# Performance work log

Measured on AMD Instinct MI355X. Metric: run time of the kernel, lower is better.

## Reference

```python
import jax, jax.numpy as jnp
from jax import lax
import numpy as np

H = 200           # mpnn_hidden_size
DEPTH = 3         # mpnn_depth
ATOM_FDIM = 39
BOND_FDIM = 11
B, NA, NB = 128, 48, 96   # molecules, atoms/mol, bonds/mol (padded fixed size)
L, VOCAB = 1000, 26       # protein length, amino-acid vocab
KERNALS = [3, 5, 7]
PROT_FILTERS = [50, 96, 128, 200]
FC_DIMS = [400, 200, 100, 1]


def setup_inputs() -> dict:
    key = jax.random.key(0)
    ks = jax.random.split(key, 32)
    s = 0.05
    inp = {}
    inp["fatoms"] = jax.random.normal(ks[0], (B, NA, ATOM_FDIM), jnp.float32)
    inp["fbonds"] = jax.random.normal(ks[1], (B, NB, ATOM_FDIM + BOND_FDIM), jnp.float32)
    inp["agraph"] = jax.random.randint(ks[2], (B, NA, 6), 0, NB)
    inp["bgraph"] = jax.random.randint(ks[3], (B, NB, 6), 0, NB)
    inp["protein_seq"] = jax.random.randint(ks[4], (B, L), 0, VOCAB)
    # MPNN weights (stored as (in, out) matrices; W_i and W_h have no bias)
    inp["W_i"] = jax.random.normal(ks[5], (ATOM_FDIM + BOND_FDIM, H), jnp.float32) * s
    inp["W_h"] = jax.random.normal(ks[6], (H, H), jnp.float32) * s
    inp["W_o_w"] = jax.random.normal(ks[7], (ATOM_FDIM + H, H), jnp.float32) * s
    inp["W_o_b"] = jax.random.normal(ks[8], (H,), jnp.float32) * s
    # protein embedding + CNN
    inp["embed_protein"] = jax.random.normal(ks[9], (VOCAB, PROT_FILTERS[0]), jnp.float32) * s
    for i, k in enumerate(KERNALS):
        inp[f"conv{i}_w"] = jax.random.normal(ks[10 + 2 * i], (PROT_FILTERS[i + 1], PROT_FILTERS[i], k), jnp.float32) * s
        inp[f"conv{i}_b"] = jax.random.normal(ks[11 + 2 * i], (PROT_FILTERS[i + 1],), jnp.float32) * s
    # CPI fc head 400 -> 200 -> 100 -> 1
    for i in range(3):
        inp[f"fc{i}_w"] = jax.random.normal(ks[16 + 2 * i], (FC_DIMS[i], FC_DIMS[i + 1]), jnp.float32) * s
        inp[f"fc{i}_b"] = jax.random.normal(ks[17 + 2 * i], (FC_DIMS[i + 1],), jnp.float32) * s
    return inp


def reference(fatoms, fbonds, agraph, bgraph, protein_seq,
              W_i, W_h, W_o_w, W_o_b, embed_protein,
              conv0_w, conv0_b, conv1_w, conv1_b, conv2_w, conv2_b,
              fc0_w, fc0_b, fc1_w, fc1_b, fc2_w, fc2_b):
    # ---- MPNN over all molecules (vmapped single_molecule_forward) ----
    def mol(fa, fb, ag, bg):
        binput = fb @ W_i                      # (NB, H)
        message = jax.nn.relu(binput)
        for _ in range(DEPTH - 1):
            nei = message[bg].sum(axis=1)      # gather (NB,6,H) -> sum -> (NB,H)
            message = jax.nn.relu(binput + nei @ W_h)
        nei = message[ag].sum(axis=1)          # (NA, H)
        atom_h = jax.nn.relu(jnp.concatenate([fa, nei], axis=1) @ W_o_w + W_o_b)
        return atom_h.mean(axis=0)             # (H,)

    embeddings = jax.vmap(mol)(fatoms, fbonds, agraph, bgraph)  # (B, H)

    # ---- protein CNN tower ----
    pv = embed_protein[protein_seq]            # (B, L, 50)
    pv = pv.transpose(0, 2, 1)                 # (B, 50, L)
    for w, b, k in ((conv0_w, conv0_b, KERNALS[0]),
                    (conv1_w, conv1_b, KERNALS[1]),
                    (conv2_w, conv2_b, KERNALS[2])):
        pv = lax.conv_general_dilated(pv, w, window_strides=(1,),
                                      padding=[(k // 2, k // 2)],
                                      dimension_numbers=("NCH", "OIH", "NCH"))
        pv = jax.nn.relu(pv + b[None, :, None])
    protein_vector = pv.max(axis=2)            # adaptive_max_pool1d(out=1) -> (B, 200)

    # ---- CPI fc head ----
    x = jnp.concatenate([embeddings, protein_vector], axis=1)  # (B, 400)
    x = jax.nn.relu(x @ fc0_w + fc0_b)
    x = jax.nn.relu(x @ fc1_w + fc1_b)
    x = x @ fc2_w + fc2_b
    return x                                   # (B, 1)
```

## Files before the change

### kernel.cpp

```cpp
#include <hip/hip_runtime.h>
#include <hip/hip_bf16.h>
#include <cstddef>

#define H 200
#define NA 48
#define NBB 96
#define BATCH 128
#define AFD 39
#define BFD 50
#define LP 1000
#define CATD (AFD + H)
#define BIPB 16
#define VOCAB 26
#define EROW 56

typedef unsigned short ushort_t;
typedef __bf16 bf16x8 __attribute__((ext_vector_type(8)));
typedef float f32x16 __attribute__((ext_vector_type(16)));
typedef unsigned uint32x4 __attribute__((ext_vector_type(4)));

union U16B { uint4 u; bf16x8 b; };
static __device__ __forceinline__ bf16x8 as_bf16x8(uint4 u) { U16B x; x.u = u; return x.b; }
union U16B2 { uint32x4 u; bf16x8 b; };
static __device__ __forceinline__ bf16x8 as_bf16x8v(uint32x4 u) { U16B2 x; x.u = u; return x.b; }

static __device__ __forceinline__ ushort_t f2bf(float f) {
    union { float f; unsigned u; } a; a.f = f;
    unsigned r = (a.u + 0x7FFFu + ((a.u >> 16) & 1u)) >> 16;
    return (ushort_t)r;
}

static __device__ __forceinline__ uint32x4 gload16(const ushort_t* base, unsigned voff) {
    uint32x4 r;
    asm volatile("global_load_dwordx4 %0, %1, %2"
                 : "=&v"(r) : "v"(voff), "s"(base));
    return r;
}

template <int COUT, int CIN, int CP, int K>
static __device__ __forceinline__ void prep_one(int t, const float* __restrict__ w,
                                                ushort_t* __restrict__ Wb) {
    constexpr int NC = CP / 16;
    constexpr int NS = K * NC;
    int j = t & 7;
    int lane = (t >> 3) & 63;
    int s = (t >> 9) % NS;
    int ct = (t >> 9) / NS;
    int co = ct * 32 + (lane & 31);
    int tt = s / NC, cc = s % NC;
    int ci = cc * 16 + ((lane >> 5) & 1) * 8 + j;
    float v = 0.f;
    if (co < COUT && ci < CIN) v = w[((size_t)co * CIN + ci) * K + tt];
    Wb[t] = f2bf(v);
}

#define MNS 13
#define ANS 15
#define PREP_T0 (4 * 12 * 512)
#define PREP_T1 (PREP_T0 + 4 * 30 * 512)
#define PREP_T2 (PREP_T1 + 8 * 56 * 512)
#define PREP_T3 (PREP_T2 + 51200)
#define PREP_T4 (PREP_T3 + 8 * MNS * 512)
#define PREP_T5 (PREP_T4 + 8 * ANS * 512)
#define PREP_T6 (PREP_T5 + VOCAB * EROW)
#define PREP_T7 (PREP_T6 + 200 * 400)
#define PREP_T8 (PREP_T7 + 100 * 200)
#define PREP_BLKS ((PREP_T8 + 255) / 256)

static __device__ __forceinline__ void prep_body(
        int tid, const float* __restrict__ c0w, const float* __restrict__ c1w,
        const float* __restrict__ c2w, const float* __restrict__ Wh,
        const float* __restrict__ Wo, const float* __restrict__ emb,
        const float* __restrict__ fc0w, const float* __restrict__ fc1w,
        float* __restrict__ x,
        ushort_t* __restrict__ Wb0, ushort_t* __restrict__ Wb1,
        ushort_t* __restrict__ Wb2, ushort_t* __restrict__ Wbh,
        ushort_t* __restrict__ Wbo, ushort_t* __restrict__ embb,
        float* __restrict__ w0t, float* __restrict__ w1t) {
    if (tid < PREP_T0) prep_one<96, 50, 64, 3>(tid, c0w, Wb0);
    else if (tid < PREP_T1) prep_one<128, 96, 96, 5>(tid - PREP_T0, c1w, Wb1);
    else if (tid < PREP_T2) prep_one<200, 128, 128, 7>(tid - PREP_T1, c2w, Wb2);
    else if (tid < PREP_T3) x[tid - PREP_T2] = 0.f;
    else if (tid < PREP_T4) {
        int t = tid - PREP_T3;
        int j = t & 7;
        int lane = (t >> 3) & 63;
        int s = (t >> 9) % MNS;
        int tile = (t >> 9) / MNS;
        int co = tile * 32 + (lane & 31);
        int ci = s * 16 + ((lane >> 5) & 1) * 8 + j;
        float v = 0.f;
        if (co < H && ci < H) v = Wh[ci * H + co];
        Wbh[t] = f2bf(v);
    } else if (tid < PREP_T5) {
        int t = tid - PREP_T4;
        int j = t & 7;
        int lane = (t >> 3) & 63;
        int s = (t >> 9) % ANS;
        int tile = (t >> 9) / ANS;
        int co = tile * 32 + (lane & 31);
        int cip = s * 16 + ((lane >> 5) & 1) * 8 + j;
        float v = 0.f;
        if (co < H) {
            if (cip < 200) v = Wo[(size_t)(39 + cip) * H + co];
            else if (cip < CATD) v = Wo[(size_t)(cip - 200) * H + co];
        }
        Wbo[t] = f2bf(v);
    } else if (tid < PREP_T6) {
        int t = tid - PREP_T5;
        int s = t / EROW, cc = t - s * EROW;
        embb[t] = (cc < 50) ? f2bf(emb[(size_t)s * 50 + cc]) : (ushort_t)0;
    } else if (tid < PREP_T7) {
        int t = tid - PREP_T6;
        int co = t % 200, k = t / 200;
        w0t[(size_t)co * 400 + k] = fc0w[(size_t)k * 200 + co];
    } else if (tid < PREP_T8) {
        int t = tid - PREP_T7;
        int co = t % 100, k = t / 100;
        w1t[(size_t)co * 200 + k] = fc1w[(size_t)k * 100 + co];
    }
}

template <int CP, int K, int COUT, int CO_WAVES, int L_WAVES, bool FMAX, bool EMB>
static __device__ __forceinline__ void conv_body(
        const ushort_t* __restrict__ act, const int* __restrict__ seq,
        const ushort_t* __restrict__ embb, const ushort_t* __restrict__ Wb,
        const float* __restrict__ bias, void* __restrict__ outv,
        ushort_t* __restrict__ Xs, int bofs) {
    constexpr int NC = CP / 16;
    constexpr int NS = K * NC;
    constexpr int P = K / 2;
    constexpr int PITCH = CP + 8;
    constexpr int LTILE = 64 * L_WAVES;
    constexpr int ROWS = LTILE + K - 1;
    constexpr int CPR = CP / 8;
    constexpr int D = 4;

    int b = blockIdx.z + bofs, lb = blockIdx.x;
    int l0 = lb * LTILE;
    int tid = threadIdx.x;

    if (EMB) {
        const int* seqb = seq + (size_t)b * LP;
        for (int idx = tid; idx < ROWS * CPR; idx += 256) {
            int r = idx / CPR, c = idx % CPR;
            int l = l0 - P + r;
            uint4 v = {0u, 0u, 0u, 0u};
            if ((unsigned)l < (unsigned)LP && c < 7) {
                int s = seqb[l];
                v = *(const uint4*)(embb + (size_t)s * EROW + c * 8);
            }
            *(uint4*)(Xs + r * PITCH + c * 8) = v;
        }
    } else {
        const ushort_t* actb = act + (size_t)b * LP * CP;
        for (int idx = tid; idx < ROWS * CPR; idx += 256) {
            int r = idx / CPR, c = idx % CPR;
            int l = l0 - P + r;
            uint4 v = {0u, 0u, 0u, 0u};
            if ((unsigned)l < (unsigned)LP)
                v = *(const uint4*)(actb + ((size_t)c * LP + l) * 8);
            *(uint4*)(Xs + r * PITCH + c * 8) = v;
        }
    }

    int lane = tid & 63, wv = tid >> 6;
    int cw = wv % CO_WAVES, lw = wv / CO_WAVES;
    int ln31 = lane & 31, half = lane >> 5;

    unsigned abase0 = (unsigned)(cw * 2) * (unsigned)NS * 1024u + (unsigned)lane * 16u;
    unsigned abase1 = abase0 + (unsigned)NS * 1024u;
    int bbase = (lw * 64 + ln31) * PITCH + half * 8;

    f32x16 acc[2][2];
#pragma unroll
    for (int ct = 0; ct < 2; ++ct)
#pragma unroll
        for (int lt = 0; lt < 2; ++lt)
#pragma unroll
            for (int r = 0; r < 16; ++r) acc[ct][lt][r] = 0.f;

    __syncthreads();

    uint32x4 ra0[D], ra1[D];
#pragma unroll
    for (int d = 0; d < D; ++d) {
        ra0[d] = gload16(Wb, abase0 + (unsigned)(d * 1024));
        ra1[d] = gload16(Wb, abase1 + (unsigned)(d * 1024));
    }

    uint4 bC0 = *(const uint4*)(Xs + bbase);
    uint4 bC1 = *(const uint4*)(Xs + bbase + 32 * PITCH);

#pragma unroll
    for (int s = 0; s < NS; ++s) {
        int sn = (s + 1 < NS) ? s + 1 : NS - 1;
        int tn = sn / NC, ccn = sn % NC;
        int off = bbase + tn * PITCH + ccn * 16;
        uint4 bN0 = *(const uint4*)(Xs + off);
        uint4 bN1 = *(const uint4*)(Xs + off + 32 * PITCH);

        {
            const int rem = NS - 1 - s;
            const int allow = 2 * ((D - 1) < rem ? (D - 1) : rem);
            asm volatile("s_waitcnt vmcnt(%0)" :: "i"(allow) : "memory");
            __builtin_amdgcn_sched_barrier(0);
        }

        uint32x4 a0 = ra0[s % D];
        uint32x4 a1 = ra1[s % D];

        acc[0][0] = __builtin_amdgcn_mfma_f32_32x32x16_bf16(
            as_bf16x8v(a0), as_bf16x8(bC0), acc[0][0], 0, 0, 0);
        acc[1][0] = __builtin_amdgcn_mfma_f32_32x32x16_bf16(
            as_bf16x8v(a1), as_bf16x8(bC0), acc[1][0], 0, 0, 0);
        acc[0][1] = __builtin_amdgcn_mfma_f32_32x32x16_bf16(
            as_bf16x8v(a0), as_bf16x8(bC1), acc[0][1], 0, 0, 0);
        acc[1][1] = __builtin_amdgcn_mfma_f32_32x32x16_bf16(
            as_bf16x8v(a1), as_bf16x8(bC1), acc[1][1], 0, 0, 0);

        if (s + D < NS) {
            ra0[s % D] = gload16(Wb, abase0 + (unsigned)((s + D) * 1024));
            ra1[s % D] = gload16(Wb, abase1 + (unsigned)((s + D) * 1024));
        }

        bC0 = bN0; bC1 = bN1;
    }

    if (!FMAX) {
        ushort_t* out = (ushort_t*)outv + (size_t)b * LP * COUT;
#pragma unroll
        for (int ct = 0; ct < 2; ++ct) {
            int cbase = (cw * 2 + ct) * 32 + 4 * half;
#pragma unroll
            for (int g = 0; g < 4; ++g) {
                int co = cbase + 8 * g;
                if (co >= COUT) continue;
                float4 bv = *(const float4*)(bias + co);
                size_t chbase = (size_t)(co >> 3) * LP;
                int sub = co & 7;
#pragma unroll
                for (int lt = 0; lt < 2; ++lt) {
                    int l = l0 + lw * 64 + lt * 32 + ln31;
                    if (l < LP) {
                        ushort_t h0 = f2bf(fmaxf(acc[ct][lt][4 * g + 0] + bv.x, 0.f));
                        ushort_t h1 = f2bf(fmaxf(acc[ct][lt][4 * g + 1] + bv.y, 0.f));
                        ushort_t h2 = f2bf(fmaxf(acc[ct][lt][4 * g + 2] + bv.z, 0.f));
                        ushort_t h3 = f2bf(fmaxf(acc[ct][lt][4 * g + 3] + bv.w, 0.f));
                        uint2 o;
                        o.x = (unsigned)h0 | ((unsigned)h1 << 16);
                        o.y = (unsigned)h2 | ((unsigned)h3 << 16);
                        *(uint2*)(out + (chbase + l) * 8 + sub) = o;
                    }
                }
            }
        }
    } else {
        float* xout = (float*)outv;
#pragma unroll
        for (int ct = 0; ct < 2; ++ct) {
            float mx[16];
#pragma unroll
            for (int r = 0; r < 16; ++r) mx[r] = -3.0e38f;
#pragma unroll
            for (int lt = 0; lt < 2; ++lt) {
                int l = l0 + lw * 64 + lt * 32 + ln31;
                if (l < LP) {
#pragma unroll
                    for (int r = 0; r < 16; ++r) mx[r] = fmaxf(mx[r], acc[ct][lt][r]);
                }
            }
#pragma unroll
            for (int r = 0; r < 16; ++r) {
#pragma unroll
                for (int off = 1; off < 32; off <<= 1)
                    mx[r] = fmaxf(mx[r], __shfl_xor(mx[r], off, 64));
            }
            if (ln31 == 0) {
                int cbase = (cw * 2 + ct) * 32 + 4 * half;
#pragma unroll
                for (int r = 0; r < 16; ++r) {
                    int co = cbase + (r & 3) + 8 * (r >> 2);
                    if (co < COUT) {
                        float v = fmaxf(mx[r] + bias[co], 0.f);
                        atomicMax((int*)&xout[(size_t)b * 400 + 200 + co], __float_as_int(v));
                    }
                }
            }
        }
    }
}

#define MPITCH 216
static __device__ __forceinline__ void msg_body(
        int blk, const float* __restrict__ msgIn, const float* __restrict__ binput,
        const int* __restrict__ bgraph, const ushort_t* __restrict__ Wbh,
        float* __restrict__ msgOut, ushort_t* __restrict__ Xs, int* __restrict__ idxs) {
    constexpr int D = 4;
    int m0 = blk * 32;
    int tid = threadIdx.x;

    if (tid < 192) {
        int r = tid / 6, j = tid - r * 6;
        int m = m0 + r;
        int mol = m / NBB;
        idxs[tid] = mol * NBB + bgraph[(size_t)m * 6 + j];
    }
    __syncthreads();

    for (int it = tid; it < 32 * 26; it += 256) {
        int r = it / 26, c = it - r * 26;
        uint4 v = {0u, 0u, 0u, 0u};
        if (c < 25) {
            float sv[8];
#pragma unroll
            for (int k = 0; k < 8; ++k) sv[k] = 0.f;
#pragma unroll
            for (int j = 0; j < 6; ++j) {
                const float* row = msgIn + (size_t)idxs[r * 6 + j] * H + c * 8;
                float4 a = *(const float4*)row;
                float4 b = *(const float4*)(row + 4);
                sv[0] += a.x; sv[1] += a.y; sv[2] += a.z; sv[3] += a.w;
                sv[4] += b.x; sv[5] += b.y; sv[6] += b.z; sv[7] += b.w;
            }
            v.x = (unsigned)f2bf(sv[0]) | ((unsigned)f2bf(sv[1]) << 16);
            v.y = (unsigned)f2bf(sv[2]) | ((unsigned)f2bf(sv[3]) << 16);
            v.z = (unsigned)f2bf(sv[4]) | ((unsigned)f2bf(sv[5]) << 16);
            v.w = (unsigned)f2bf(sv[6]) | ((unsigned)f2bf(sv[7]) << 16);
        }
        *(uint4*)(Xs + r * MPITCH + c * 8) = v;
    }

    int lane = tid & 63, wv = tid >> 6;
    int ln31 = lane & 31, half = lane >> 5;
    unsigned abase0 = (unsigned)(wv * 2) * (unsigned)MNS * 1024u + (unsigned)lane * 16u;
    unsigned abase1 = abase0 + (unsigned)MNS * 1024u;
    int bbase = ln31 * MPITCH + half * 8;

    f32x16 acc[2];
#pragma unroll
    for (int ct = 0; ct < 2; ++ct)
#pragma unroll
        for (int r = 0; r < 16; ++r) acc[ct][r] = 0.f;

    __syncthreads();

    uint32x4 ra0[4], ra1[4];
#pragma unroll
    for (int d = 0; d < D; ++d) {
        ra0[d] = gload16(Wbh, abase0 + (unsigned)(d * 1024));
        ra1[d] = gload16(Wbh, abase1 + (unsigned)(d * 1024));
    }

    uint4 bC = *(const uint4*)(Xs + bbase);

#pragma unroll
    for (int s = 0; s < MNS; ++s) {
        int sn = (s + 1 < MNS) ? s + 1 : MNS - 1;
        uint4 bN = *(const uint4*)(Xs + bbase + sn * 16);

        {
            const int rem = MNS - 1 - s;
            const int allow = 2 * ((D - 1) < rem ? (D - 1) : rem);
            asm volatile("s_waitcnt vmcnt(%0)" :: "i"(allow) : "memory");
            __builtin_amdgcn_sched_barrier(0);
        }

        uint32x4 a0 = ra0[s % D];
        uint32x4 a1 = ra1[s % D];
        acc[0] = __builtin_amdgcn_mfma_f32_32x32x16_bf16(
            as_bf16x8v(a0), as_bf16x8(bC), acc[0], 0, 0, 0);
        acc[1] = __builtin_amdgcn_mfma_f32_32x32x16_bf16(
            as_bf16x8v(a1), as_bf16x8(bC), acc[1], 0, 0, 0);

        if (s + D < MNS) {
            ra0[s % D] = gload16(Wbh, abase0 + (unsigned)((s + D) * 1024));
            ra1[s % D] = gload16(Wbh, abase1 + (unsigned)((s + D) * 1024));
        }
        bC = bN;
    }

    int m = m0 + ln31;
    const float* bi = binput + (size_t)m * H;
    float* outp = msgOut + (size_t)m * H;
#pragma unroll
    for (int ct = 0; ct < 2; ++ct) {
        int cbase = (wv * 2 + ct) * 32 + 4 * half;
#pragma unroll
        for (int g = 0; g < 4; ++g) {
            int co = cbase + 8 * g;
            if (co >= H) continue;
            float4 b4 = *(const float4*)(bi + co);
            float4 o;
            o.x = fmaxf(acc[ct][4 * g + 0] + b4.x, 0.f);
            o.y = fmaxf(acc[ct][4 * g + 1] + b4.y, 0.f);
            o.z = fmaxf(acc[ct][4 * g + 2] + b4.z, 0.f);
            o.w = fmaxf(acc[ct][4 * g + 3] + b4.w, 0.f);
            *(float4*)(outp + co) = o;
        }
    }
}

#define APITCH 248
static __device__ __forceinline__ void atom_mfma_body(
        int blk, const float* __restrict__ msg, const float* __restrict__ fatoms,
        const int* __restrict__ agraph, const ushort_t* __restrict__ Wbo,
        const float* __restrict__ Wob, float* __restrict__ x,
        ushort_t* __restrict__ Xs, int* __restrict__ idxs) {
    constexpr int D = 4;
    int m0 = blk * 32;
    int tid = threadIdx.x;

    if (tid < 192) {
        int r = tid / 6, j = tid - r * 6;
        int m = m0 + r;
        int mol = m / NA;
        idxs[tid] = mol * NBB + agraph[(size_t)m * 6 + j];
    }
    __syncthreads();

    for (int it = tid; it < 32 * 30; it += 256) {
        int r = it / 30, c = it - r * 30;
        uint4 v = {0u, 0u, 0u, 0u};
        if (c < 25) {
            float sv[8];
#pragma unroll
            for (int k = 0; k < 8; ++k) sv[k] = 0.f;
#pragma unroll
            for (int j = 0; j < 6; ++j) {
                const float* row = msg + (size_t)idxs[r * 6 + j] * H + c * 8;
                float4 a = *(const float4*)row;
                float4 b = *(const float4*)(row + 4);
                sv[0] += a.x; sv[1] += a.y; sv[2] += a.z; sv[3] += a.w;
                sv[4] += b.x; sv[5] += b.y; sv[6] += b.z; sv[7] += b.w;
            }
            v.x = (unsigned)f2bf(sv[0]) | ((unsigned)f2bf(sv[1]) << 16);
            v.y = (unsigned)f2bf(sv[2]) | ((unsigned)f2bf(sv[3]) << 16);
            v.z = (unsigned)f2bf(sv[4]) | ((unsigned)f2bf(sv[5]) << 16);
            v.w = (unsigned)f2bf(sv[6]) | ((unsigned)f2bf(sv[7]) << 16);
        } else {
            int m = m0 + r;
            ushort_t h[8];
#pragma unroll
            for (int j = 0; j < 8; ++j) {
                int f = c * 8 + j - 200;
                h[j] = (f < AFD) ? f2bf(fatoms[(size_t)m * AFD + f]) : (ushort_t)0;
            }
            v.x = (unsigned)h[0] | ((unsigned)h[1] << 16);
            v.y = (unsigned)h[2] | ((unsigned)h[3] << 16);
            v.z = (unsigned)h[4] | ((unsigned)h[5] << 16);
            v.w = (unsigned)h[6] | ((unsigned)h[7] << 16);
        }
        *(uint4*)(Xs + r * APITCH + c * 8) = v;
    }

    int lane = tid & 63, wv = tid >> 6;
    int ln31 = lane & 31, half = lane >> 5;
    unsigned abase0 = (unsigned)(wv * 2) * (unsigned)ANS * 1024u + (unsigned)lane * 16u;
    unsigned abase1 = abase0 + (unsigned)ANS * 1024u;
    int bbase = ln31 * APITCH + half * 8;

    f32x16 acc[2];
#pragma unroll
    for (int ct = 0; ct < 2; ++ct)
#pragma unroll
        for (int r = 0; r < 16; ++r) acc[ct][r] = 0.f;

    __syncthreads();

    uint32x4 ra0[4], ra1[4];
#pragma unroll
    for (int d = 0; d < D; ++d) {
        ra0[d] = gload16(Wbo, abase0 + (unsigned)(d * 1024));
        ra1[d] = gload16(Wbo, abase1 + (unsigned)(d * 1024));
    }

    uint4 bC = *(const uint4*)(Xs + bbase);

#pragma unroll
    for (int s = 0; s < ANS; ++s) {
        int sn = (s + 1 < ANS) ? s + 1 : ANS - 1;
        uint4 bN = *(const uint4*)(Xs + bbase + sn * 16);

        {
            const int rem = ANS - 1 - s;
            const int allow = 2 * ((D - 1) < rem ? (D - 1) : rem);
            asm volatile("s_waitcnt vmcnt(%0)" :: "i"(allow) : "memory");
            __builtin_amdgcn_sched_barrier(0);
        }

        uint32x4 a0 = ra0[s % D];
        uint32x4 a1 = ra1[s % D];
        acc[0] = __builtin_amdgcn_mfma_f32_32x32x16_bf16(
            as_bf16x8v(a0), as_bf16x8(bC), acc[0], 0, 0, 0);
        acc[1] = __builtin_amdgcn_mfma_f32_32x32x16_bf16(
            as_bf16x8v(a1), as_bf16x8(bC), acc[1], 0, 0, 0);

        if (s + D < ANS) {
            ra0[s % D] = gload16(Wbo, abase0 + (unsigned)((s + D) * 1024));
            ra1[s % D] = gload16(Wbo, abase1 + (unsigned)((s + D) * 1024));
        }
        bC = bN;
    }

    int rm = m0 % 48;
    bool split = (rm == 32);
    int molA = m0 / 48;
    const float inv = 1.f / NA;
#pragma unroll
    for (int ct = 0; ct < 2; ++ct) {
        int cbase = (wv * 2 + ct) * 32 + 4 * half;
#pragma unroll
        for (int r = 0; r < 16; ++r) {
            int co = cbase + (r & 3) + 8 * (r >> 2);
            float v = 0.f;
            if (co < H) v = fmaxf(acc[ct][r] + Wob[co], 0.f) * inv;
            v += __shfl_xor(v, 1, 64);
            v += __shfl_xor(v, 2, 64);
            v += __shfl_xor(v, 4, 64);
            v += __shfl_xor(v, 8, 64);
            if (!split) v += __shfl_xor(v, 16, 64);
            if (co < H) {
                if (ln31 == 0) atomicAdd(&x[(size_t)molA * 400 + co], v);
                else if (split && ln31 == 16) atomicAdd(&x[(size_t)(molA + 1) * 400 + co], v);
            }
        }
    }
}

static __device__ __forceinline__ void bond_body(
        int blk, const float* __restrict__ fbonds, const float* __restrict__ Wi,
        float* __restrict__ binput, float* __restrict__ msg, float (*fb)[BFD]) {
    int bond0 = blk * BIPB;
    int tid = threadIdx.x;
    for (int idx = tid; idx < BIPB * BFD; idx += 256)
        fb[idx / BFD][idx % BFD] = fbonds[(size_t)bond0 * BFD + idx];
    __syncthreads();
    if (tid < H) {
        float acc[BIPB];
#pragma unroll
        for (int q = 0; q < BIPB; ++q) acc[q] = 0.f;
#pragma unroll 5
        for (int k = 0; k < BFD; ++k) {
            float w = Wi[k * H + tid];
#pragma unroll
            for (int q = 0; q < BIPB; ++q) acc[q] += fb[q][k] * w;
        }
#pragma unroll
        for (int q = 0; q < BIPB; ++q) {
            size_t o = (size_t)(bond0 + q) * H + tid;
            binput[o] = acc[q];
            msg[o] = fmaxf(acc[q], 0.f);
        }
    }
}


__global__ __launch_bounds__(256) void k_l0_prep_bond(
        const float* __restrict__ c0w, const float* __restrict__ c1w,
        const float* __restrict__ c2w, const float* __restrict__ Wh,
        const float* __restrict__ Wo, const float* __restrict__ emb,
        const float* __restrict__ fc0w, const float* __restrict__ fc1w,
        float* __restrict__ x,
        ushort_t* __restrict__ Wb0, ushort_t* __restrict__ Wb1,
        ushort_t* __restrict__ Wb2, ushort_t* __restrict__ Wbh,
        ushort_t* __restrict__ Wbo, ushort_t* __restrict__ embb,
        float* __restrict__ w0t, float* __restrict__ w1t,
        const float* __restrict__ fbonds, const float* __restrict__ Wi,
        float* __restrict__ binput, float* __restrict__ msgA) {
    __shared__ float fb[BIPB][BFD];
    int bid = blockIdx.x;
    if (bid < PREP_BLKS) {
        prep_body(bid * 256 + threadIdx.x, c0w, c1w, c2w, Wh, Wo, emb, fc0w, fc1w, x,
                  Wb0, Wb1, Wb2, Wbh, Wbo, embb, w0t, w1t);
    } else {
        bond_body(bid - PREP_BLKS, fbonds, Wi, binput, msgA, fb);
    }
}

__global__ __launch_bounds__(256, 4) void k_l1_conv0_msg(
        const int* __restrict__ seq, const ushort_t* __restrict__ embb,
        const ushort_t* __restrict__ Wb0, const float* __restrict__ c0b,
        ushort_t* __restrict__ act1,
        const float* __restrict__ msgIn, const float* __restrict__ binput,
        const int* __restrict__ bgraph, const ushort_t* __restrict__ Wbh,
        float* __restrict__ msgOut) {
    __shared__ __align__(16) ushort_t Sbuf[(128 + 2) * (64 + 8)];
    if (blockIdx.x < 8) {
        conv_body<64, 3, 96, 2, 2, false, true>(nullptr, seq, embb, Wb0, c0b, act1, Sbuf, 0);
    } else {
        int blk = (blockIdx.x - 8) * 128 + blockIdx.z;
        msg_body(blk, msgIn, binput, bgraph, Wbh, msgOut, Sbuf,
                 (int*)(Sbuf + 32 * MPITCH));
    }
}

__global__ __launch_bounds__(256, 4) void k_l2_conv1_msg(
        const ushort_t* __restrict__ act1, const ushort_t* __restrict__ Wb1,
        const float* __restrict__ c1b, ushort_t* __restrict__ act2,
        const float* __restrict__ msgIn, const float* __restrict__ binput,
        const int* __restrict__ bgraph, const ushort_t* __restrict__ Wbh,
        float* __restrict__ msgOut) {
    __shared__ __align__(16) ushort_t Sbuf[(128 + 4) * (96 + 8)];
    if (blockIdx.x < 8) {
        conv_body<96, 5, 128, 2, 2, false, false>(act1, nullptr, nullptr, Wb1, c1b, act2,
                                                  Sbuf, 0);
    } else {
        int blk = (blockIdx.x - 8) * 128 + blockIdx.z;
        msg_body(blk, msgIn, binput, bgraph, Wbh, msgOut, Sbuf,
                 (int*)(Sbuf + 32 * MPITCH));
    }
}

__global__ __launch_bounds__(256, 4) void k_conv2(
        const ushort_t* __restrict__ act2, const ushort_t* __restrict__ Wb2,
        const float* __restrict__ c2b, float* __restrict__ x) {
    __shared__ __align__(16) ushort_t Xs[(64 + 6) * (128 + 8)];
    conv_body<128, 7, 200, 4, 1, true, false>(act2, nullptr, nullptr, Wb2, c2b, x, Xs, 0);
}

__global__ __launch_bounds__(256, 4) void k_atom_mfma(
        const float* __restrict__ msg, const float* __restrict__ fatoms,
        const int* __restrict__ agraph, const ushort_t* __restrict__ Wbo,
        const float* __restrict__ Wob, float* __restrict__ x) {
    __shared__ __align__(16) ushort_t Xs[32 * APITCH];
    __shared__ int idxs[192];
    atom_mfma_body(blockIdx.x, msg, fatoms, agraph, Wbo, Wob, x, Xs, idxs);
}

__global__ __launch_bounds__(512) void k_fc(
        const float* __restrict__ x,
        const float* __restrict__ w0t, const float* __restrict__ b0,
        const float* __restrict__ w1t, const float* __restrict__ b1,
        const float* __restrict__ w2, const float* __restrict__ b2,
        float* __restrict__ out) {
    int b = blockIdx.x, tid = threadIdx.x;
    int lane = tid & 63, wv = tid >> 6;
    __shared__ __align__(16) float xr[400];
    __shared__ __align__(16) float h1[200];
    __shared__ __align__(16) float h2[100];
    for (int i = tid; i < 400; i += 512) xr[i] = x[(size_t)b * 400 + i];
    __syncthreads();
    for (int o = 0; o < 25; ++o) {
        int co = wv * 25 + o;
        const float* wr = w0t + (size_t)co * 400;
        int k0 = lane * 4;
        float4 wa = *(const float4*)(wr + k0);
        float4 xa = *(const float4*)(xr + k0);
        float s = wa.x * xa.x + wa.y * xa.y + wa.z * xa.z + wa.w * xa.w;
        int k1 = 256 + lane * 4;
        if (k1 < 400) {
            float4 wb = *(const float4*)(wr + k1);
            float4 xb = *(const float4*)(xr + k1);
            s += wb.x * xb.x + wb.y * xb.y + wb.z * xb.z + wb.w * xb.w;
        }
#pragma unroll
        for (int off = 1; off < 64; off <<= 1) s += __shfl_xor(s, off, 64);
        if (lane == 0) h1[co] = fmaxf(s + b0[co], 0.f);
    }
    __syncthreads();
    if (wv < 4) {
        for (int o = 0; o < 25; ++o) {
            int co = wv * 25 + o;
            const float* wr = w1t + (size_t)co * 200;
            float s = 0.f;
            int k0 = lane * 4;
            if (k0 < 200) {
                float4 wa = *(const float4*)(wr + k0);
                float4 xa = *(const float4*)(h1 + k0);
                s = wa.x * xa.x + wa.y * xa.y + wa.z * xa.z + wa.w * xa.w;
            }
#pragma unroll
            for (int off = 1; off < 64; off <<= 1) s += __shfl_xor(s, off, 64);
            if (lane == 0) h2[co] = fmaxf(s + b1[co], 0.f);
        }
    }
    __syncthreads();
    if (wv == 0) {
        float s = 0.f;
        int k0 = lane * 4;
        if (k0 < 100) {
            float4 wa = *(const float4*)(w2 + k0);
            float4 xa = *(const float4*)(h2 + k0);
            s = wa.x * xa.x + wa.y * xa.y + wa.z * xa.z + wa.w * xa.w;
        }
#pragma unroll
        for (int off = 1; off < 64; off <<= 1) s += __shfl_xor(s, off, 64);
        if (lane == 0) out[b] = s + b2[0];
    }
}

extern "C" void kernel_launch(void* const* d_in, const int* in_sizes, int n_in,
                              void* d_out, int out_size, void* d_ws, size_t ws_size,
                              hipStream_t stream) {
    const float* fatoms = (const float*)d_in[0];
    const float* fbonds = (const float*)d_in[1];
    const int* agraph = (const int*)d_in[2];
    const int* bgraph = (const int*)d_in[3];
    const int* seq = (const int*)d_in[4];
    const float* Wi = (const float*)d_in[5];
    const float* Wh = (const float*)d_in[6];
    const float* Wo = (const float*)d_in[7];
    const float* Wob = (const float*)d_in[8];
    const float* embp = (const float*)d_in[9];
    const float* c0w = (const float*)d_in[10];
    const float* c0b = (const float*)d_in[11];
    const float* c1w = (const float*)d_in[12];
    const float* c1b = (const float*)d_in[13];
    const float* c2w = (const float*)d_in[14];
    const float* c2b = (const float*)d_in[15];
    const float* fc0w = (const float*)d_in[16];
    const float* fc0b = (const float*)d_in[17];
    const float* fc1w = (const float*)d_in[18];
    const float* fc1b = (const float*)d_in[19];
    const float* fc2w = (const float*)d_in[20];
    const float* fc2b = (const float*)d_in[21];

    float* ws = (float*)d_ws;
    float* binput = ws;
    float* msgA = binput + 2457600;
    float* msgB = msgA + 2457600;
    float* x = msgB + 2457600;
    ushort_t* u = (ushort_t*)(x + 51200);
    ushort_t* act1 = u;
    ushort_t* act2 = act1 + 12288000;
    ushort_t* Wb0 = act2 + 16384000;
    ushort_t* Wb1 = Wb0 + 24576;
    ushort_t* Wb2 = Wb1 + 61440;
    ushort_t* Wbh = Wb2 + 229376;
    ushort_t* Wbo = Wbh + 53248;
    ushort_t* embb = Wbo + 61440;
    float* w0t = (float*)(embb + 1456);
    float* w1t = w0t + 200 * 400;

    k_l0_prep_bond<<<PREP_BLKS + BATCH * NBB / BIPB, 256, 0, stream>>>(
        c0w, c1w, c2w, Wh, Wo, embp, fc0w, fc1w, x, Wb0, Wb1, Wb2, Wbh, Wbo, embb,
        w0t, w1t, fbonds, Wi, binput, msgA);

    k_l1_conv0_msg<<<dim3(8 + 3, 1, BATCH), 256, 0, stream>>>(
        seq, embb, Wb0, c0b, act1, msgA, binput, bgraph, Wbh, msgB);

    k_l2_conv1_msg<<<dim3(8 + 3, 1, BATCH), 256, 0, stream>>>(
        act1, Wb1, c1b, act2, msgB, binput, bgraph, Wbh, msgA);

    k_conv2<<<dim3(16, 1, BATCH), 256, 0, stream>>>(act2, Wb2, c2b, x);

    k_atom_mfma<<<BATCH * NA / 32, 256, 0, stream>>>(msgA, fatoms, agraph, Wbo, Wob, x);

    k_fc<<<BATCH, 512, 0, stream>>>(x, w0t, fc0b, w1t, fc1b, fc2w, fc2b, (float*)d_out);
}
```

Measured before the change: 306.1 us.

## Split fused conv/message-passing kernels into separate conv and msg launches

Conv layers and MPNN message steps previously ran as heterogeneous blocks inside one launch, so they could overlap. They now run as four separate kernels on the same stream, each sizing its own shared memory. This removes branch divergence between block types and lets the small msg kernels use less LDS, which may raise occupancy. In exchange the two independent workloads now run back to back, which adds two extra launches and gives up the concurrency between them.

```diff
diff --git a/kernel.cpp b/kernel.cpp
--- a/kernel.cpp
+++ b/kernel.cpp
@@ -578,38 +578,37 @@
     }
 }
 
-__global__ __launch_bounds__(256, 4) void k_l1_conv0_msg(
+__global__ __launch_bounds__(256, 4) void k_conv0(
         const int* __restrict__ seq, const ushort_t* __restrict__ embb,
         const ushort_t* __restrict__ Wb0, const float* __restrict__ c0b,
-        ushort_t* __restrict__ act1,
+        ushort_t* __restrict__ act1) {
+    __shared__ __align__(16) ushort_t Xs[(128 + 2) * (64 + 8)];
+    conv_body<64, 3, 96, 2, 2, false, true>(nullptr, seq, embb, Wb0, c0b, act1, Xs, 0);
+}
+
+__global__ __launch_bounds__(256, 4) void k_msg1(
         const float* __restrict__ msgIn, const float* __restrict__ binput,
         const int* __restrict__ bgraph, const ushort_t* __restrict__ Wbh,
         float* __restrict__ msgOut) {
-    __shared__ __align__(16) ushort_t Sbuf[(128 + 2) * (64 + 8)];
-    if (blockIdx.x < 8) {
-        conv_body<64, 3, 96, 2, 2, false, true>(nullptr, seq, embb, Wb0, c0b, act1, Sbuf, 0);
-    } else {
-        int blk = (blockIdx.x - 8) * 128 + blockIdx.z;
-        msg_body(blk, msgIn, binput, bgraph, Wbh, msgOut, Sbuf,
-                 (int*)(Sbuf + 32 * MPITCH));
-    }
-}
-
-__global__ __launch_bounds__(256, 4) void k_l2_conv1_msg(
+    __shared__ __align__(16) ushort_t Xs[32 * MPITCH];
+    __shared__ int idxs[192];
+    msg_body(blockIdx.x, msgIn, binput, bgraph, Wbh, msgOut, Xs, idxs);
+}
+
+__global__ __launch_bounds__(256, 4) void k_conv1(
         const ushort_t* __restrict__ act1, const ushort_t* __restrict__ Wb1,
-        const float* __restrict__ c1b, ushort_t* __restrict__ act2,
+        const float* __restrict__ c1b, ushort_t* __restrict__ act2) {
+    __shared__ __align__(16) ushort_t Xs[(128 + 4) * (96 + 8)];
+    conv_body<96, 5, 128, 2, 2, false, false>(act1, nullptr, nullptr, Wb1, c1b, act2, Xs, 0);
+}
+
+__global__ __launch_bounds__(256, 4) void k_msg2(
         const float* __restrict__ msgIn, const float* __restrict__ binput,
         const int* __restrict__ bgraph, const ushort_t* __restrict__ Wbh,
         float* __restrict__ msgOut) {
-    __shared__ __align__(16) ushort_t Sbuf[(128 + 4) * (96 + 8)];
-    if (blockIdx.x < 8) {
-        conv_body<96, 5, 128, 2, 2, false, false>(act1, nullptr, nullptr, Wb1, c1b, act2,
-                                                  Sbuf, 0);
-    } else {
-        int blk = (blockIdx.x - 8) * 128 + blockIdx.z;
-        msg_body(blk, msgIn, binput, bgraph, Wbh, msgOut, Sbuf,
-                 (int*)(Sbuf + 32 * MPITCH));
-    }
+    __shared__ __align__(16) ushort_t Xs[32 * MPITCH];
+    __shared__ int idxs[192];
+    msg_body(blockIdx.x, msgIn, binput, bgraph, Wbh, msgOut, Xs, idxs);
 }
 
 __global__ __launch_bounds__(256, 4) void k_conv2(
@@ -737,11 +736,10 @@
         c0w, c1w, c2w, Wh, Wo, embp, fc0w, fc1w, x, Wb0, Wb1, Wb2, Wbh, Wbo, embb,
         w0t, w1t, fbonds, Wi, binput, msgA);
 
-    k_l1_conv0_msg<<<dim3(8 + 3, 1, BATCH), 256, 0, stream>>>(
-        seq, embb, Wb0, c0b, act1, msgA, binput, bgraph, Wbh, msgB);
-
-    k_l2_conv1_msg<<<dim3(8 + 3, 1, BATCH), 256, 0, stream>>>(
-        act1, Wb1, c1b, act2, msgB, binput, bgraph, Wbh, msgA);
+    k_conv0<<<dim3(8, 1, BATCH), 256, 0, stream>>>(seq, embb, Wb0, c0b, act1);
+    k_msg1<<<BATCH * NBB / 32, 256, 0, stream>>>(msgA, binput, bgraph, Wbh, msgB);
+    k_conv1<<<dim3(8, 1, BATCH), 256, 0, stream>>>(act1, Wb1, c1b, act2);
+    k_msg2<<<BATCH * NBB / 32, 256, 0, stream>>>(msgB, binput, bgraph, Wbh, msgA);
 
     k_conv2<<<dim3(16, 1, BATCH), 256, 0, stream>>>(act2, Wb2, c2b, x);
 
```

New measurement: 305.7 us. About the same (-0.1%).
